# Kernel tuning notes

Measured on AMD Instinct MI355X. Metric: run time of the kernel, lower is better.

The kernel has to match this reference:

```python
import jax, jax.numpy as jnp
import numpy as np


def setup_inputs() -> dict:
    key = jax.random.key(0)
    ks = jax.random.split(key, 9)
    B, N, E = 4, 100000, 400000
    Dv = De = Dc = 64
    Din, H, Dout = De + 2 * Dv + Dc, 128, 64  # 256, 128, 64
    return {
        "vdata": jax.random.normal(ks[0], (B, N, Dv), dtype=jnp.float32),
        "edata": jax.random.normal(ks[1], (B, E, De), dtype=jnp.float32),
        "cdata": jax.random.normal(ks[2], (B, Dc), dtype=jnp.float32),
        "W1": jax.random.normal(ks[3], (Din, H), dtype=jnp.float32) * (1.0 / np.sqrt(Din)),
        "b1": jnp.zeros((H,), dtype=jnp.float32),
        "W2": jax.random.normal(ks[4], (H, Dout), dtype=jnp.float32) * (1.0 / np.sqrt(H)),
        "b2": jnp.zeros((Dout,), dtype=jnp.float32),
        "sender_ids": jax.random.randint(ks[5], (B, E), 0, N, dtype=jnp.int64 if jax.config.jax_enable_x64 else jnp.int32).astype(jnp.int32),
        "receiver_ids": jax.random.randint(ks[6], (B, E), 0, N, dtype=jnp.int64 if jax.config.jax_enable_x64 else jnp.int32).astype(jnp.int32),
    }


def reference(vdata, edata, cdata, W1, b1, W2, b2, sender_ids, receiver_ids):
    # Gather sender/receiver vertex features per edge: [B,E,Dv]
    gather = jax.vmap(lambda v, idx: v[idx])  # per-graph gather along node dim
    sender_data = gather(vdata, sender_ids)
    receiver_data = gather(vdata, receiver_ids)
    B, E = edata.shape[0], edata.shape[1]
    # Context repeated per edge: [B,E,Dc]
    ctx = jnp.broadcast_to(cdata[:, None, :], (B, E, cdata.shape[-1]))
    # etin = cat(edge, sender, receiver, context) along feature dim -> [B,E,256]
    etin = jnp.concatenate([edata, sender_data, receiver_data, ctx], axis=2)
    # Batched MLP updater
    h = jax.nn.relu(jnp.einsum("bei,ih->beh", etin, W1) + b1)
    out = jnp.einsum("beh,ho->beo", h, W2) + b2
    return out
```

## Files before the change

kernel.cpp:

```cpp
#include <hip/hip_runtime.h>

typedef __attribute__((ext_vector_type(8))) __bf16 bf16x8;
typedef __attribute__((ext_vector_type(4))) float f32x4;
typedef __attribute__((ext_vector_type(4))) unsigned int u32x4;

#define NBATCH 4
#define NV 100000
#define NE 400000
#define DIN 256
#define HID 128
#define DOUT 64

#define W1T_OFF 0
#define W2T_OFF 65536
#define HB_OFF  81920
#define B1_OFF  147456
#define B2_OFF  147968
#define LDS_SIZE 148224

__device__ inline unsigned short f2b_rne(float f) {
    unsigned u = __builtin_bit_cast(unsigned, f);
    return (unsigned short)((u + 0x7fffu + ((u >> 16) & 1u)) >> 16);
}

__device__ inline bf16x8 pack8(f32x4 a, f32x4 b) {
    unsigned r0, r1, r2, r3;
    asm("v_cvt_pk_bf16_f32 %0, %1, %2" : "=v"(r0) : "v"(a[0]), "v"(a[1]));
    asm("v_cvt_pk_bf16_f32 %0, %1, %2" : "=v"(r1) : "v"(a[2]), "v"(a[3]));
    asm("v_cvt_pk_bf16_f32 %0, %1, %2" : "=v"(r2) : "v"(b[0]), "v"(b[1]));
    asm("v_cvt_pk_bf16_f32 %0, %1, %2" : "=v"(r3) : "v"(b[2]), "v"(b[3]));
    u32x4 u = {r0, r1, r2, r3};
    return __builtin_bit_cast(bf16x8, u);
}

__device__ inline bf16x8 load8(const float* p) {
    f32x4 x = *(const f32x4*)p;
    f32x4 y = *(const f32x4*)(p + 4);
    return pack8(x, y);
}

__global__ __launch_bounds__(512, 2) void edgeblock_kernel(
    const float* __restrict__ vdata, const float* __restrict__ edata,
    const float* __restrict__ cdata, const float* __restrict__ W1,
    const float* __restrict__ b1, const float* __restrict__ W2,
    const float* __restrict__ b2, const int* __restrict__ snd,
    const int* __restrict__ rcv, float* __restrict__ out)
{
    __shared__ __align__(16) unsigned char lds[LDS_SIZE];
    const int tid = threadIdx.x;
    const int lane = tid & 63;
    const int w = tid >> 6;
    const int l15 = lane & 15;
    const int lg = lane >> 4;

    const int b   = blockIdx.x >> 6;
    const int blk = blockIdx.x & 63;

    for (int i = tid; i < DIN * HID; i += 512) {
        int k = i >> 7, n = i & 127;
        unsigned short h = f2b_rne(W1[i]);
        *(unsigned short*)(lds + W1T_OFF + n * 512 + ((k * 2) ^ ((n & 7) << 4))) = h;
    }
    for (int i = tid; i < HID * DOUT; i += 512) {
        int k = i >> 6, n = i & 63;
        unsigned short h = f2b_rne(W2[i]);
        *(unsigned short*)(lds + W2T_OFF + n * 256 + ((k * 2) ^ ((n & 7) << 4))) = h;
    }
    if (tid < HID)  *(float*)(lds + B1_OFF + tid * 4) = b1[tid];
    if (tid < DOUT) *(float*)(lds + B2_OFF + tid * 4) = b2[tid];
    __syncthreads();

    float b1v[8], b2v[4];
#pragma unroll
    for (int n = 0; n < 8; ++n) b1v[n] = *(const float*)(lds + B1_OFF + (n * 16 + l15) * 4);
#pragma unroll
    for (int n = 0; n < 4; ++n) b2v[n] = *(const float*)(lds + B2_OFF + (n * 16 + l15) * 4);

    const float* cd = cdata + b * 64;
    bf16x8 cfr0 = load8(cd + lg * 8);
    bf16x8 cfr1 = load8(cd + 32 + lg * 8);

    const size_t bE = (size_t)b * NE;
    const float* ed_b = edata + bE * 64;
    const float* vd_b = vdata + (size_t)b * NV * 64;
    const int* snd_b = snd + bE;
    const int* rcv_b = rcv + bE;
    float* out_b = out + bE * 64;
    unsigned char* hb = lds + HB_OFF + w * 8192;

    const int n_tiles = NE / 32;
    for (int t = blk * 8 + w; t < n_tiles; t += 512) {
        const int e0 = t * 32;

        int sid0 = snd_b[e0 + l15], sid1 = snd_b[e0 + 16 + l15];
        int rid0 = rcv_b[e0 + l15], rid1 = rcv_b[e0 + 16 + l15];

        bf16x8 a[2][8];
        {
            const float* erow0 = ed_b + (size_t)(e0 + l15) * 64;
            const float* erow1 = ed_b + (size_t)(e0 + 16 + l15) * 64;
            const float* srow0 = vd_b + (size_t)sid0 * 64;
            const float* srow1 = vd_b + (size_t)sid1 * 64;
            const float* rrow0 = vd_b + (size_t)rid0 * 64;
            const float* rrow1 = vd_b + (size_t)rid1 * 64;
            const int c0 = lg * 8;
            a[0][0] = load8(erow0 + c0);      a[0][1] = load8(erow0 + 32 + c0);
            a[0][2] = load8(srow0 + c0);      a[0][3] = load8(srow0 + 32 + c0);
            a[0][4] = load8(rrow0 + c0);      a[0][5] = load8(rrow0 + 32 + c0);
            a[0][6] = cfr0;                   a[0][7] = cfr1;
            a[1][0] = load8(erow1 + c0);      a[1][1] = load8(erow1 + 32 + c0);
            a[1][2] = load8(srow1 + c0);      a[1][3] = load8(srow1 + 32 + c0);
            a[1][4] = load8(rrow1 + c0);      a[1][5] = load8(rrow1 + 32 + c0);
            a[1][6] = cfr0;                   a[1][7] = cfr1;
        }

        f32x4 acc[2][8];
#pragma unroll
        for (int mt = 0; mt < 2; ++mt)
#pragma unroll
            for (int n = 0; n < 8; ++n) { f32x4 z = {0.f, 0.f, 0.f, 0.f}; acc[mt][n] = z; }

#pragma unroll
        for (int n = 0; n < 8; ++n) {
            const int row = n * 16 + l15;
            const unsigned char* wrow = lds + W1T_OFF + row * 512;
            const int swz = (row & 7) << 4;
#pragma unroll
            for (int kk = 0; kk < 8; ++kk) {
                bf16x8 bf = *(const bf16x8*)(wrow + ((kk * 64 + lg * 16) ^ swz));
                acc[0][n] = __builtin_amdgcn_mfma_f32_16x16x32_bf16(a[0][kk], bf, acc[0][n], 0, 0, 0);
                acc[1][n] = __builtin_amdgcn_mfma_f32_16x16x32_bf16(a[1][kk], bf, acc[1][n], 0, 0, 0);
            }
        }

#pragma unroll
        for (int mt = 0; mt < 2; ++mt)
#pragma unroll
            for (int n = 0; n < 8; ++n)
#pragma unroll
                for (int r = 0; r < 4; ++r) {
                    int row = mt * 16 + lg * 4 + r;
                    int col = n * 16 + l15;
                    float hv = fmaxf(acc[mt][n][r] + b1v[n], 0.f);
                    *(unsigned short*)(hb + row * 256 + ((col * 2) ^ ((row & 7) << 4))) = f2b_rne(hv);
                }

        bf16x8 ha[2][4];
#pragma unroll
        for (int mt = 0; mt < 2; ++mt) {
            const int row = mt * 16 + l15;
            const int swz = (row & 7) << 4;
#pragma unroll
            for (int kk = 0; kk < 4; ++kk)
                ha[mt][kk] = *(const bf16x8*)(hb + row * 256 + ((kk * 64 + lg * 16) ^ swz));
        }

        f32x4 acc2[2][4];
#pragma unroll
        for (int mt = 0; mt < 2; ++mt)
#pragma unroll
            for (int nt = 0; nt < 4; ++nt) { f32x4 z = {0.f, 0.f, 0.f, 0.f}; acc2[mt][nt] = z; }

#pragma unroll
        for (int nt = 0; nt < 4; ++nt) {
            const int rw = nt * 16 + l15;
            const unsigned char* wrow = lds + W2T_OFF + rw * 256;
            const int swz = (rw & 7) << 4;
#pragma unroll
            for (int kk = 0; kk < 4; ++kk) {
                bf16x8 bf = *(const bf16x8*)(wrow + ((kk * 64 + lg * 16) ^ swz));
                acc2[0][nt] = __builtin_amdgcn_mfma_f32_16x16x32_bf16(ha[0][kk], bf, acc2[0][nt], 0, 0, 0);
                acc2[1][nt] = __builtin_amdgcn_mfma_f32_16x16x32_bf16(ha[1][kk], bf, acc2[1][nt], 0, 0, 0);
            }
        }

#pragma unroll
        for (int mt = 0; mt < 2; ++mt)
#pragma unroll
            for (int nt = 0; nt < 4; ++nt)
#pragma unroll
                for (int r = 0; r < 4; ++r) {
                    int e = e0 + mt * 16 + lg * 4 + r;
                    out_b[(size_t)e * 64 + nt * 16 + l15] = acc2[mt][nt][r] + b2v[nt];
                }
    }
}

extern "C" void kernel_launch(void* const* d_in, const int* in_sizes, int n_in,
                              void* d_out, int out_size, void* d_ws, size_t ws_size,
                              hipStream_t stream) {
    const float* vdata = (const float*)d_in[0];
    const float* edata = (const float*)d_in[1];
    const float* cdata = (const float*)d_in[2];
    const float* W1    = (const float*)d_in[3];
    const float* b1    = (const float*)d_in[4];
    const float* W2    = (const float*)d_in[5];
    const float* b2    = (const float*)d_in[6];
    const int*   snd   = (const int*)d_in[7];
    const int*   rcv   = (const int*)d_in[8];
    float* out = (float*)d_out;

    edgeblock_kernel<<<dim3(256), dim3(512), 0, stream>>>(
        vdata, edata, cdata, W1, b1, W2, b2, snd, rcv, out);
}
```

Measured before the change: 336.1 us.

## Swap MFMA operands to keep hidden activations in registers and drop LDS staging

Computes the transposed product (weights as A operand, edge features as B) so the first GEMM's accumulator layout can be repacked directly into bf16 B fragments for the second GEMM. W2 is stored in LDS with a permuted k order to match that layout, which removes the per-wave hidden-activation LDS buffer and its scalar stores and loads. Biases are folded into the accumulator initialisation, and outputs are written as 16-byte vectors instead of scalars. The smaller LDS footprint lets the kernel raise its occupancy hint and launch twice as many blocks, and edge-row loads are software-pipelined one k-chunk ahead. The cost is the bespoke W2 permutation, which has to match the accumulator layout exactly.

Result: slower. 403.4 us (+20.0%).

```diff
diff --git a/kernel.cpp b/kernel.cpp
--- a/kernel.cpp
+++ b/kernel.cpp
@@ -4,32 +4,26 @@
 typedef __attribute__((ext_vector_type(4))) float f32x4;
 typedef __attribute__((ext_vector_type(4))) unsigned int u32x4;
 
-#define NBATCH 4
 #define NV 100000
 #define NE 400000
-#define DIN 256
-#define HID 128
-#define DOUT 64
 
 #define W1T_OFF 0
 #define W2T_OFF 65536
-#define HB_OFF  81920
-#define B1_OFF  147456
-#define B2_OFF  147968
-#define LDS_SIZE 148224
+#define LDS_SIZE 81920
 
 __device__ inline unsigned short f2b_rne(float f) {
     unsigned u = __builtin_bit_cast(unsigned, f);
     return (unsigned short)((u + 0x7fffu + ((u >> 16) & 1u)) >> 16);
 }
 
+__device__ inline unsigned pk2(float lo, float hi) {
+    unsigned r;
+    asm("v_cvt_pk_bf16_f32 %0, %1, %2" : "=v"(r) : "v"(lo), "v"(hi));
+    return r;
+}
+
 __device__ inline bf16x8 pack8(f32x4 a, f32x4 b) {
-    unsigned r0, r1, r2, r3;
-    asm("v_cvt_pk_bf16_f32 %0, %1, %2" : "=v"(r0) : "v"(a[0]), "v"(a[1]));
-    asm("v_cvt_pk_bf16_f32 %0, %1, %2" : "=v"(r1) : "v"(a[2]), "v"(a[3]));
-    asm("v_cvt_pk_bf16_f32 %0, %1, %2" : "=v"(r2) : "v"(b[0]), "v"(b[1]));
-    asm("v_cvt_pk_bf16_f32 %0, %1, %2" : "=v"(r3) : "v"(b[2]), "v"(b[3]));
-    u32x4 u = {r0, r1, r2, r3};
+    u32x4 u = {pk2(a[0], a[1]), pk2(a[2], a[3]), pk2(b[0], b[1]), pk2(b[2], b[3])};
     return __builtin_bit_cast(bf16x8, u);
 }
 
@@ -39,7 +33,7 @@
     return pack8(x, y);
 }
 
-__global__ __launch_bounds__(512, 2) void edgeblock_kernel(
+__global__ __launch_bounds__(512, 4) void edgeblock_kernel(
     const float* __restrict__ vdata, const float* __restrict__ edata,
     const float* __restrict__ cdata, const float* __restrict__ W1,
     const float* __restrict__ b1, const float* __restrict__ W2,
@@ -53,32 +47,26 @@
     const int l15 = lane & 15;
     const int lg = lane >> 4;
 
-    const int b   = blockIdx.x >> 6;
-    const int blk = blockIdx.x & 63;
+    const int b   = blockIdx.x >> 7;
+    const int blk = blockIdx.x & 127;
 
-    for (int i = tid; i < DIN * HID; i += 512) {
+    for (int i = tid; i < 256 * 128; i += 512) {
         int k = i >> 7, n = i & 127;
-        unsigned short h = f2b_rne(W1[i]);
-        *(unsigned short*)(lds + W1T_OFF + n * 512 + ((k * 2) ^ ((n & 7) << 4))) = h;
+        *(unsigned short*)(lds + W1T_OFF + n * 512 + ((k * 2) ^ ((n & 7) << 4))) = f2b_rne(W1[i]);
     }
-    for (int i = tid; i < HID * DOUT; i += 512) {
+    for (int i = tid; i < 128 * 64; i += 512) {
         int k = i >> 6, n = i & 63;
-        unsigned short h = f2b_rne(W2[i]);
-        *(unsigned short*)(lds + W2T_OFF + n * 256 + ((k * 2) ^ ((n & 7) << 4))) = h;
+        int kc2 = k >> 5, c = k & 31;
+        int j   = ((c >> 4) << 2) | (c & 3);
+        int lgs = (c >> 2) & 3;
+        int off = kc2 * 64 + lgs * 16 + j * 2;
+        *(unsigned short*)(lds + W2T_OFF + n * 256 + (off ^ ((n & 7) << 4))) = f2b_rne(W2[i]);
     }
-    if (tid < HID)  *(float*)(lds + B1_OFF + tid * 4) = b1[tid];
-    if (tid < DOUT) *(float*)(lds + B2_OFF + tid * 4) = b2[tid];
     __syncthreads();
 
-    float b1v[8], b2v[4];
-#pragma unroll
-    for (int n = 0; n < 8; ++n) b1v[n] = *(const float*)(lds + B1_OFF + (n * 16 + l15) * 4);
-#pragma unroll
-    for (int n = 0; n < 4; ++n) b2v[n] = *(const float*)(lds + B2_OFF + (n * 16 + l15) * 4);
-
     const float* cd = cdata + b * 64;
-    bf16x8 cfr0 = load8(cd + lg * 8);
-    bf16x8 cfr1 = load8(cd + 32 + lg * 8);
+    const bf16x8 cfr0 = load8(cd + lg * 8);
+    const bf16x8 cfr1 = load8(cd + 32 + lg * 8);
 
     const size_t bE = (size_t)b * NE;
     const float* ed_b = edata + bE * 64;
@@ -86,103 +74,87 @@
     const int* snd_b = snd + bE;
     const int* rcv_b = rcv + bE;
     float* out_b = out + bE * 64;
-    unsigned char* hb = lds + HB_OFF + w * 8192;
 
-    const int n_tiles = NE / 32;
-    for (int t = blk * 8 + w; t < n_tiles; t += 512) {
+    for (int t = blk * 8 + w; t < NE / 32; t += 1024) {
         const int e0 = t * 32;
+        const int sid0 = snd_b[e0 + l15],      sid1 = snd_b[e0 + 16 + l15];
+        const int rid0 = rcv_b[e0 + l15],      rid1 = rcv_b[e0 + 16 + l15];
+        const float* rows0[3] = { ed_b + (size_t)(e0 + l15) * 64,
+                                  vd_b + (size_t)sid0 * 64,
+                                  vd_b + (size_t)rid0 * 64 };
+        const float* rows1[3] = { ed_b + (size_t)(e0 + 16 + l15) * 64,
+                                  vd_b + (size_t)sid1 * 64,
+                                  vd_b + (size_t)rid1 * 64 };
 
-        int sid0 = snd_b[e0 + l15], sid1 = snd_b[e0 + 16 + l15];
-        int rid0 = rcv_b[e0 + l15], rid1 = rcv_b[e0 + 16 + l15];
-
-        bf16x8 a[2][8];
-        {
-            const float* erow0 = ed_b + (size_t)(e0 + l15) * 64;
-            const float* erow1 = ed_b + (size_t)(e0 + 16 + l15) * 64;
-            const float* srow0 = vd_b + (size_t)sid0 * 64;
-            const float* srow1 = vd_b + (size_t)sid1 * 64;
-            const float* rrow0 = vd_b + (size_t)rid0 * 64;
-            const float* rrow1 = vd_b + (size_t)rid1 * 64;
-            const int c0 = lg * 8;
-            a[0][0] = load8(erow0 + c0);      a[0][1] = load8(erow0 + 32 + c0);
-            a[0][2] = load8(srow0 + c0);      a[0][3] = load8(srow0 + 32 + c0);
-            a[0][4] = load8(rrow0 + c0);      a[0][5] = load8(rrow0 + 32 + c0);
-            a[0][6] = cfr0;                   a[0][7] = cfr1;
-            a[1][0] = load8(erow1 + c0);      a[1][1] = load8(erow1 + 32 + c0);
-            a[1][2] = load8(srow1 + c0);      a[1][3] = load8(srow1 + 32 + c0);
-            a[1][4] = load8(rrow1 + c0);      a[1][5] = load8(rrow1 + 32 + c0);
-            a[1][6] = cfr0;                   a[1][7] = cfr1;
+        f32x4 acc1[8][2];
+#pragma unroll
+        for (int ht = 0; ht < 8; ++ht) {
+            f32x4 bv = *(const f32x4*)(b1 + ht * 16 + lg * 4);
+            acc1[ht][0] = bv; acc1[ht][1] = bv;
         }
 
-        f32x4 acc[2][8];
+        bf16x8 bc0 = load8(rows0[0] + lg * 8);
+        bf16x8 bc1 = load8(rows1[0] + lg * 8);
 #pragma unroll
-        for (int mt = 0; mt < 2; ++mt)
+        for (int kc = 0; kc < 8; ++kc) {
+            bf16x8 bn0, bn1;
+            if (kc < 7) {
+                const int kn = kc + 1;
+                if (kn >= 6) { bn0 = (kn & 1) ? cfr1 : cfr0; bn1 = bn0; }
+                else {
+                    bn0 = load8(rows0[kn >> 1] + (kn & 1) * 32 + lg * 8);
+                    bn1 = load8(rows1[kn >> 1] + (kn & 1) * 32 + lg * 8);
+                }
+            }
 #pragma unroll
-            for (int n = 0; n < 8; ++n) { f32x4 z = {0.f, 0.f, 0.f, 0.f}; acc[mt][n] = z; }
-
-#pragma unroll
-        for (int n = 0; n < 8; ++n) {
-            const int row = n * 16 + l15;
-            const unsigned char* wrow = lds + W1T_OFF + row * 512;
-            const int swz = (row & 7) << 4;
-#pragma unroll
-            for (int kk = 0; kk < 8; ++kk) {
-                bf16x8 bf = *(const bf16x8*)(wrow + ((kk * 64 + lg * 16) ^ swz));
-                acc[0][n] = __builtin_amdgcn_mfma_f32_16x16x32_bf16(a[0][kk], bf, acc[0][n], 0, 0, 0);
-                acc[1][n] = __builtin_amdgcn_mfma_f32_16x16x32_bf16(a[1][kk], bf, acc[1][n], 0, 0, 0);
+            for (int ht = 0; ht < 8; ++ht) {
+                const int row = ht * 16 + l15;
+                const bf16x8 wf = *(const bf16x8*)(lds + W1T_OFF + row * 512 +
+                                                   ((kc * 64 + lg * 16) ^ ((row & 7) << 4)));
+                acc1[ht][0] = __builtin_amdgcn_mfma_f32_16x16x32_bf16(wf, bc0, acc1[ht][0], 0, 0, 0);
+                acc1[ht][1] = __builtin_amdgcn_mfma_f32_16x16x32_bf16(wf, bc1, acc1[ht][1], 0, 0, 0);
             }
+            if (kc < 7) { bc0 = bn0; bc1 = bn1; }
         }
 
+        bf16x8 q[2][4];
 #pragma unroll
-        for (int mt = 0; mt < 2; ++mt)
+        for (int kc2 = 0; kc2 < 4; ++kc2)
 #pragma unroll
-            for (int n = 0; n < 8; ++n)
+            for (int et = 0; et < 2; ++et) {
+                f32x4 u = acc1[2 * kc2][et], v = acc1[2 * kc2 + 1][et];
+                u32x4 pq;
+                pq[0] = pk2(fmaxf(u[0], 0.f), fmaxf(u[1], 0.f));
+                pq[1] = pk2(fmaxf(u[2], 0.f), fmaxf(u[3], 0.f));
+                pq[2] = pk2(fmaxf(v[0], 0.f), fmaxf(v[1], 0.f));
+                pq[3] = pk2(fmaxf(v[2], 0.f), fmaxf(v[3], 0.f));
+                q[et][kc2] = __builtin_bit_cast(bf16x8, pq);
+            }
+
+        f32x4 acc2[4][2];
 #pragma unroll
-                for (int r = 0; r < 4; ++r) {
-                    int row = mt * 16 + lg * 4 + r;
-                    int col = n * 16 + l15;
-                    float hv = fmaxf(acc[mt][n][r] + b1v[n], 0.f);
-                    *(unsigned short*)(hb + row * 256 + ((col * 2) ^ ((row & 7) << 4))) = f2b_rne(hv);
-                }
+        for (int dt = 0; dt < 4; ++dt) {
+            f32x4 bv = *(const f32x4*)(b2 + dt * 16 + lg * 4);
+            acc2[dt][0] = bv; acc2[dt][1] = bv;
+        }
+#pragma unroll
+        for (int kc2 = 0; kc2 < 4; ++kc2)
+#pragma unroll
+            for (int dt = 0; dt < 4; ++dt) {
+                const int row = dt * 16 + l15;
+                const bf16x8 wf = *(const bf16x8*)(lds + W2T_OFF + row * 256 +
+                                                   ((kc2 * 64 + lg * 16) ^ ((row & 7) << 4)));
+                acc2[dt][0] = __builtin_amdgcn_mfma_f32_16x16x32_bf16(wf, q[0][kc2], acc2[dt][0], 0, 0, 0);
+                acc2[dt][1] = __builtin_amdgcn_mfma_f32_16x16x32_bf16(wf, q[1][kc2], acc2[dt][1], 0, 0, 0);
+            }
 
-        bf16x8 ha[2][4];
+        float* ob0 = out_b + (size_t)(e0 + l15) * 64 + lg * 4;
+        float* ob1 = out_b + (size_t)(e0 + 16 + l15) * 64 + lg * 4;
 #pragma unroll
-        for (int mt = 0; mt < 2; ++mt) {
-            const int row = mt * 16 + l15;
-            const int swz = (row & 7) << 4;
-#pragma unroll
-            for (int kk = 0; kk < 4; ++kk)
-                ha[mt][kk] = *(const bf16x8*)(hb + row * 256 + ((kk * 64 + lg * 16) ^ swz));
+        for (int dt = 0; dt < 4; ++dt) {
+            *(f32x4*)(ob0 + dt * 16) = acc2[dt][0];
+            *(f32x4*)(ob1 + dt * 16) = acc2[dt][1];
         }
-
-        f32x4 acc2[2][4];
-#pragma unroll
-        for (int mt = 0; mt < 2; ++mt)
-#pragma unroll
-            for (int nt = 0; nt < 4; ++nt) { f32x4 z = {0.f, 0.f, 0.f, 0.f}; acc2[mt][nt] = z; }
-
-#pragma unroll
-        for (int nt = 0; nt < 4; ++nt) {
-            const int rw = nt * 16 + l15;
-            const unsigned char* wrow = lds + W2T_OFF + rw * 256;
-            const int swz = (rw & 7) << 4;
-#pragma unroll
-            for (int kk = 0; kk < 4; ++kk) {
-                bf16x8 bf = *(const bf16x8*)(wrow + ((kk * 64 + lg * 16) ^ swz));
-                acc2[0][nt] = __builtin_amdgcn_mfma_f32_16x16x32_bf16(ha[0][kk], bf, acc2[0][nt], 0, 0, 0);
-                acc2[1][nt] = __builtin_amdgcn_mfma_f32_16x16x32_bf16(ha[1][kk], bf, acc2[1][nt], 0, 0, 0);
-            }
-        }
-
-#pragma unroll
-        for (int mt = 0; mt < 2; ++mt)
-#pragma unroll
-            for (int nt = 0; nt < 4; ++nt)
-#pragma unroll
-                for (int r = 0; r < 4; ++r) {
-                    int e = e0 + mt * 16 + lg * 4 + r;
-                    out_b[(size_t)e * 64 + nt * 16 + l15] = acc2[mt][nt][r] + b2v[nt];
-                }
     }
 }
 
@@ -200,6 +172,6 @@
     const int*   rcv   = (const int*)d_in[8];
     float* out = (float*)d_out;
 
-    edgeblock_kernel<<<dim3(256), dim3(512), 0, stream>>>(
+    edgeblock_kernel<<<dim3(512), dim3(512), 0, stream>>>(
         vdata, edata, cdata, W1, b1, W2, b2, snd, rcv, out);
 }
```
